# Performance work log

Measured on AMD Instinct MI355X. Metric: run time of the kernel, lower is better.

Reference implementation:

```python
import jax, jax.numpy as jnp
import numpy as np

B, T, C, H, L, V = 4, 1024, 768, 12, 6, 50257
HS = C // H
FF = 4 * C
NEG = jnp.float32(-1e9)


def setup_inputs() -> dict:
    key = jax.random.key(0)
    ks = jax.random.split(key, 16)
    n = lambda k, shape: jax.random.normal(k, shape, jnp.float32) * 0.02
    return {
        "idx": jax.random.randint(ks[0], (B, T), 0, V),
        "targets": jax.random.randint(ks[1], (B, T), 0, V),
        "tok_emb": n(ks[2], (V, C)),
        "pos_emb": n(ks[3], (T, C)),  # block_size == T
        "Wq": n(ks[4], (L, C, C)), "Wk": n(ks[5], (L, C, C)), "Wv": n(ks[6], (L, C, C)),
        "Wp": n(ks[7], (L, C, C)), "bp": jnp.zeros((L, C), jnp.float32),
        "ln1_g": jnp.ones((L, C), jnp.float32), "ln1_b": jnp.zeros((L, C), jnp.float32),
        "ln2_g": jnp.ones((L, C), jnp.float32), "ln2_b": jnp.zeros((L, C), jnp.float32),
        "W1": n(ks[8], (L, C, FF)), "b1": jnp.zeros((L, FF), jnp.float32),
        "W2": n(ks[9], (L, FF, C)), "b2": jnp.zeros((L, C), jnp.float32),
        "lnf_g": jnp.ones((C,), jnp.float32), "lnf_b": jnp.zeros((C,), jnp.float32),
        "Wh": n(ks[10], (C, V)), "bh": jnp.zeros((V,), jnp.float32),
    }


def _ln(x, g, b):
    m = x.mean(-1, keepdims=True)
    v = x.var(-1, keepdims=True)
    return (x - m) * jax.lax.rsqrt(v + 1e-5) * g + b


def reference(idx, targets, tok_emb, pos_emb, Wq, Wk, Wv, Wp, bp,
              ln1_g, ln1_b, ln2_g, ln2_b, W1, b1, W2, b2,
              lnf_g, lnf_b, Wh, bh):
    x = tok_emb[idx] + pos_emb[:T]                       # (B,T,C)
    mask = jnp.tril(jnp.ones((T, T), bool))              # causal tril buffer
    scale = jnp.float32(HS) ** -0.5
    for l in range(L):
        h = _ln(x, ln1_g[l], ln1_b[l])
        q = (h @ Wq[l]).reshape(B, T, H, HS)
        k = (h @ Wk[l]).reshape(B, T, H, HS)
        v = (h @ Wv[l]).reshape(B, T, H, HS)
        wei = jnp.einsum('bihd,bjhd->bhij', q, k) * scale
        wei = jnp.where(mask, wei, NEG)
        wei = jax.nn.softmax(wei, axis=-1)               # dropout is eval no-op
        att = jnp.einsum('bhij,bjhd->bihd', wei, v).reshape(B, T, C)
        x = x + att @ Wp[l] + bp[l]
        h2 = _ln(x, ln2_g[l], ln2_b[l])
        x = x + jax.nn.relu(h2 @ W1[l] + b1[l]) @ W2[l] + b2[l]
    x = _ln(x, lnf_g, lnf_b)
    logits = x @ Wh + bh                                  # (B,T,V)
    logp = jax.nn.log_softmax(logits.reshape(B * T, V), axis=-1)
    nll = -jnp.take_along_axis(logp, targets.reshape(B * T, 1), axis=1)
    loss = nll.mean()
    return logits, loss
```

## Files before the change

kernel.cpp:

```cpp
#include <hip/hip_runtime.h>
#include <hip/hip_bf16.h>

#define DI __device__ __forceinline__

typedef __bf16 bf16_t;
typedef __bf16 bf16x8 __attribute__((ext_vector_type(8)));
typedef float f32x4 __attribute__((ext_vector_type(4)));

static constexpr int Bc = 4, Tc = 1024, Cc = 768, Hc = 12, Lc = 6, Vc = 50257;
static constexpr int FFc = 3072, BT = Bc * Tc;
static constexpr int Vpad = 50304;
static constexpr int NPAN = Vpad / 128;

DI void gld_lds16(const void* g, void* l) {
  __builtin_amdgcn_global_load_lds((__attribute__((address_space(1))) void*)(void*)g,
                                   (__attribute__((address_space(3))) void*)l, 16, 0, 0);
}
DI bf16_t f2b(float v) { return (bf16_t)v; }
DI unsigned short b2u(bf16_t h) { union { bf16_t b; unsigned short u; } x; x.b = h; return x.u; }

__global__ void tconv(const float* __restrict__ src, bf16_t* __restrict__ dst,
                      const int K, const int N, const long sStride, const long dStride) {
  __shared__ float t[32][33];
  src += (long)blockIdx.z * sStride;
  dst += (long)blockIdx.z * dStride;
  const int n0 = blockIdx.x * 32, k0 = blockIdx.y * 32;
  const int tr = threadIdx.x >> 5, tc = threadIdx.x & 31;
#pragma unroll
  for (int i = 0; i < 4; ++i) {
    const int n = n0 + tc;
    t[tr + i * 8][tc] = (n < N) ? src[(long)(k0 + tr + i * 8) * N + n] : 0.f;
  }
  __syncthreads();
#pragma unroll
  for (int i = 0; i < 4; ++i)
    dst[(long)(n0 + tr + i * 8) * K + k0 + tc] = f2b(t[tc][tr + i * 8]);
}

__global__ void embed_ln(const int* __restrict__ idx, const float* __restrict__ tok,
                         const float* __restrict__ pos, const float* __restrict__ g,
                         const float* __restrict__ b, float* __restrict__ X,
                         bf16_t* __restrict__ out) {
  const int lane = threadIdx.x & 63;
  const long row = (long)blockIdx.x * 4 + (threadIdx.x >> 6);
  const int t = (int)(row & (Tc - 1));
  const float* tr = tok + (long)idx[row] * Cc;
  const float* pr = pos + (long)t * Cc;
  float v[12];
  float s = 0.f;
#pragma unroll
  for (int i = 0; i < 3; ++i) {
    const int c = lane * 4 + i * 256;
    const float4 a = *(const float4*)(tr + c);
    const float4 p = *(const float4*)(pr + c);
    float4 x;
    x.x = a.x + p.x; x.y = a.y + p.y; x.z = a.z + p.z; x.w = a.w + p.w;
    *(float4*)(X + row * Cc + c) = x;
    v[i * 4 + 0] = x.x; v[i * 4 + 1] = x.y; v[i * 4 + 2] = x.z; v[i * 4 + 3] = x.w;
    s += x.x + x.y + x.z + x.w;
  }
#pragma unroll
  for (int o = 1; o < 64; o <<= 1) s += __shfl_xor(s, o);
  const float mean = s * (1.f / 768.f);
  float q = 0.f;
#pragma unroll
  for (int j = 0; j < 12; ++j) { const float d = v[j] - mean; q += d * d; }
#pragma unroll
  for (int o = 1; o < 64; o <<= 1) q += __shfl_xor(q, o);
  const float rstd = rsqrtf(q * (1.f / 768.f) + 1e-5f);
#pragma unroll
  for (int i = 0; i < 3; ++i) {
    const int c = lane * 4 + i * 256;
    const float4 gg = *(const float4*)(g + c);
    const float4 bb = *(const float4*)(b + c);
    ushort4 o4;
    o4.x = b2u(f2b((v[i * 4 + 0] - mean) * rstd * gg.x + bb.x));
    o4.y = b2u(f2b((v[i * 4 + 1] - mean) * rstd * gg.y + bb.y));
    o4.z = b2u(f2b((v[i * 4 + 2] - mean) * rstd * gg.z + bb.z));
    o4.w = b2u(f2b((v[i * 4 + 3] - mean) * rstd * gg.w + bb.w));
    *(ushort4*)(out + row * Cc + c) = o4;
  }
}

__global__ void ln_k(const float* __restrict__ x, const float* __restrict__ g,
                     const float* __restrict__ b, bf16_t* __restrict__ out) {
  const int lane = threadIdx.x & 63;
  const long row = (long)blockIdx.x * 4 + (threadIdx.x >> 6);
  const float* xr = x + row * Cc;
  float v[12];
  float s = 0.f;
#pragma unroll
  for (int i = 0; i < 3; ++i) {
    const float4 f = *(const float4*)(xr + lane * 4 + i * 256);
    v[i * 4 + 0] = f.x; v[i * 4 + 1] = f.y; v[i * 4 + 2] = f.z; v[i * 4 + 3] = f.w;
    s += f.x + f.y + f.z + f.w;
  }
#pragma unroll
  for (int o = 1; o < 64; o <<= 1) s += __shfl_xor(s, o);
  const float mean = s * (1.f / 768.f);
  float q = 0.f;
#pragma unroll
  for (int j = 0; j < 12; ++j) { const float d = v[j] - mean; q += d * d; }
#pragma unroll
  for (int o = 1; o < 64; o <<= 1) q += __shfl_xor(q, o);
  const float rstd = rsqrtf(q * (1.f / 768.f) + 1e-5f);
#pragma unroll
  for (int i = 0; i < 3; ++i) {
    const int c = lane * 4 + i * 256;
    const float4 gg = *(const float4*)(g + c);
    const float4 bb = *(const float4*)(b + c);
    ushort4 o4;
    o4.x = b2u(f2b((v[i * 4 + 0] - mean) * rstd * gg.x + bb.x));
    o4.y = b2u(f2b((v[i * 4 + 1] - mean) * rstd * gg.y + bb.y));
    o4.z = b2u(f2b((v[i * 4 + 2] - mean) * rstd * gg.z + bb.z));
    o4.w = b2u(f2b((v[i * 4 + 3] - mean) * rstd * gg.w + bb.w));
    *(ushort4*)(out + row * Cc + c) = o4;
  }
}

__global__ void red_ln(const float* __restrict__ P, const float* __restrict__ bias,
                       const float* __restrict__ g, const float* __restrict__ b,
                       float* __restrict__ X, bf16_t* __restrict__ out) {
  const int lane = threadIdx.x & 63;
  const long row = (long)blockIdx.x * 4 + (threadIdx.x >> 6);
  float v[12];
  float s = 0.f;
#pragma unroll
  for (int i = 0; i < 3; ++i) {
    const int c = lane * 4 + i * 256;
    const float4 x0 = *(const float4*)(X + row * Cc + c);
    const float4 p0 = *(const float4*)(P + row * Cc + c);
    const float4 p1 = *(const float4*)(P + (size_t)BT * Cc + row * Cc + c);
    const float4 bb = *(const float4*)(bias + c);
    float4 x;
    x.x = x0.x + p0.x + p1.x + bb.x;
    x.y = x0.y + p0.y + p1.y + bb.y;
    x.z = x0.z + p0.z + p1.z + bb.z;
    x.w = x0.w + p0.w + p1.w + bb.w;
    *(float4*)(X + row * Cc + c) = x;
    v[i * 4 + 0] = x.x; v[i * 4 + 1] = x.y; v[i * 4 + 2] = x.z; v[i * 4 + 3] = x.w;
    s += x.x + x.y + x.z + x.w;
  }
#pragma unroll
  for (int o = 1; o < 64; o <<= 1) s += __shfl_xor(s, o);
  const float mean = s * (1.f / 768.f);
  float q = 0.f;
#pragma unroll
  for (int j = 0; j < 12; ++j) { const float d = v[j] - mean; q += d * d; }
#pragma unroll
  for (int o = 1; o < 64; o <<= 1) q += __shfl_xor(q, o);
  const float rstd = rsqrtf(q * (1.f / 768.f) + 1e-5f);
#pragma unroll
  for (int i = 0; i < 3; ++i) {
    const int c = lane * 4 + i * 256;
    const float4 gg = *(const float4*)(g + c);
    const float4 bb = *(const float4*)(b + c);
    ushort4 o4;
    o4.x = b2u(f2b((v[i * 4 + 0] - mean) * rstd * gg.x + bb.x));
    o4.y = b2u(f2b((v[i * 4 + 1] - mean) * rstd * gg.y + bb.y));
    o4.z = b2u(f2b((v[i * 4 + 2] - mean) * rstd * gg.z + bb.z));
    o4.w = b2u(f2b((v[i * 4 + 3] - mean) * rstd * gg.w + bb.w));
    *(ushort4*)(out + row * Cc + c) = o4;
  }
}

template <int EPI>
__launch_bounds__(256, 4)
__global__ void gemm_bt(const bf16_t* __restrict__ A, const bf16_t* __restrict__ Bt,
                        const float* __restrict__ bias, bf16_t* __restrict__ outB,
                        float* __restrict__ resid, float* __restrict__ fpart,
                        const int N, const int K, const int ldk, const int ldo) {
  __shared__ __align__(16) bf16_t As[128 * 64];
  __shared__ __align__(16) bf16_t Bs[128 * 64];
  const int tid = threadIdx.x;
  const int lane = tid & 63, wid = tid >> 6;
  const int l4 = lane >> 4, l15 = lane & 15;
  const int wr = wid >> 1, wc = wid & 1;

  int flat;
  {
    const int nwg = gridDim.x * gridDim.y;
    int f = (int)blockIdx.y * gridDim.x + (int)blockIdx.x;
    const int q = nwg >> 3, r = nwg & 7;
    const int xcd = f & 7, pos = f >> 3;
    flat = (xcd < r) ? xcd * (q + 1) + pos : r * (q + 1) + (xcd - r) * q + pos;
  }
  const long m0 = (long)(flat / gridDim.x) * 128;
  const long n0 = (long)(flat % gridDim.x) * 128;
  const long koff = (long)blockIdx.z * K;

  const bf16_t* Ag = A + m0 * ldk + koff;
  const bf16_t* Bg = Bt + n0 * ldk + koff;
  const int srow = tid >> 3, scol = tid & 7;

  f32x4 acc[4][4];
#pragma unroll
  for (int m = 0; m < 4; ++m)
#pragma unroll
    for (int n = 0; n < 4; ++n) acc[m][n] = (f32x4){0.f, 0.f, 0.f, 0.f};

  const int nkt = K >> 6;
  for (int kt = 0; kt < nkt; ++kt) {
    const int kb = kt << 6;
#pragma unroll
    for (int i = 0; i < 4; ++i) {
      const int r_ = i * 32 + srow;
      const int c8 = scol ^ (r_ & 7);
      gld_lds16(Ag + (long)r_ * ldk + kb + c8 * 8, As + (i * 256 + tid) * 8);
      gld_lds16(Bg + (long)r_ * ldk + kb + c8 * 8, Bs + (i * 256 + tid) * 8);
    }
    __syncthreads();
#pragma unroll
    for (int kk = 0; kk < 2; ++kk) {
      bf16x8 af[4], bfv[4];
#pragma unroll
      for (int m = 0; m < 4; ++m) {
        const int row = wr * 64 + m * 16 + l15;
        af[m] = *(const bf16x8*)((const char*)As +
                 ((row * 128 + kk * 64 + l4 * 16) ^ ((row & 7) << 4)));
      }
#pragma unroll
      for (int n = 0; n < 4; ++n) {
        const int row = wc * 64 + n * 16 + l15;
        bfv[n] = *(const bf16x8*)((const char*)Bs +
                 ((row * 128 + kk * 64 + l4 * 16) ^ ((row & 7) << 4)));
      }
#pragma unroll
      for (int m = 0; m < 4; ++m)
#pragma unroll
        for (int n = 0; n < 4; ++n)
          acc[m][n] = __builtin_amdgcn_mfma_f32_16x16x32_bf16(af[m], bfv[n], acc[m][n], 0, 0, 0);
    }
    __syncthreads();
  }

#pragma unroll
  for (int m = 0; m < 4; ++m) {
    const long rowb = m0 + wr * 64 + m * 16 + l4 * 4;
#pragma unroll
    for (int n = 0; n < 4; ++n) {
      const int col = (int)n0 + wc * 64 + n * 16 + l15;
#pragma unroll
      for (int r = 0; r < 4; ++r) {
        const float v = acc[m][n][r];
        const long row = rowb + r;
        if constexpr (EPI == 0) {
          outB[row * ldo + col] = f2b(v);
        } else if constexpr (EPI == 1) {
          const float z = v + bias[col];
          outB[row * ldo + col] = f2b(z > 0.f ? z : 0.f);
        } else if constexpr (EPI == 2) {
          resid[row * ldo + col] += v + bias[col];
        } else {
          fpart[((size_t)blockIdx.z * BT + row) * ldo + col] = v;
        }
      }
    }
  }
}

__launch_bounds__(256, 4)
__global__ void head_k(const bf16_t* __restrict__ A, const bf16_t* __restrict__ Bt,
                       const float* __restrict__ bias, float* __restrict__ outF,
                       const int K, const int ldo, float* __restrict__ part1) {
  __shared__ __align__(16) bf16_t As[128 * 64];
  __shared__ __align__(16) bf16_t Bs[128 * 64];
  const int tid = threadIdx.x;
  const int lane = tid & 63, wid = tid >> 6;
  const int l4 = lane >> 4, l15 = lane & 15;
  const int wr = wid >> 1, wc = wid & 1;
  const long m0 = (long)blockIdx.y * 128;
  const long n0 = (long)blockIdx.x * 128;

  const bf16_t* Ag = A + m0 * K;
  const bf16_t* Bg = Bt + n0 * K;
  const int srow = tid >> 3, scol = tid & 7;

  f32x4 acc[4][4];
#pragma unroll
  for (int m = 0; m < 4; ++m)
#pragma unroll
    for (int n = 0; n < 4; ++n) acc[m][n] = (f32x4){0.f, 0.f, 0.f, 0.f};

  const int nkt = K >> 6;
  for (int kt = 0; kt < nkt; ++kt) {
    const int kb = kt << 6;
#pragma unroll
    for (int i = 0; i < 4; ++i) {
      const int r_ = i * 32 + srow;
      const int c8 = scol ^ (r_ & 7);
      gld_lds16(Ag + (long)r_ * K + kb + c8 * 8, As + (i * 256 + tid) * 8);
      gld_lds16(Bg + (long)r_ * K + kb + c8 * 8, Bs + (i * 256 + tid) * 8);
    }
    __syncthreads();
#pragma unroll
    for (int kk = 0; kk < 2; ++kk) {
      bf16x8 af[4], bfv[4];
#pragma unroll
      for (int m = 0; m < 4; ++m) {
        const int row = wr * 64 + m * 16 + l15;
        af[m] = *(const bf16x8*)((const char*)As +
                 ((row * 128 + kk * 64 + l4 * 16) ^ ((row & 7) << 4)));
      }
#pragma unroll
      for (int n = 0; n < 4; ++n) {
        const int row = wc * 64 + n * 16 + l15;
        bfv[n] = *(const bf16x8*)((const char*)Bs +
                 ((row * 128 + kk * 64 + l4 * 16) ^ ((row & 7) << 4)));
      }
#pragma unroll
      for (int m = 0; m < 4; ++m)
#pragma unroll
        for (int n = 0; n < 4; ++n)
          acc[m][n] = __builtin_amdgcn_mfma_f32_16x16x32_bf16(af[m], bfv[n], acc[m][n], 0, 0, 0);
    }
    __syncthreads();
  }

  float* ps = (float*)&As[0];
#pragma unroll
  for (int m = 0; m < 4; ++m)
#pragma unroll
    for (int r = 0; r < 4; ++r) {
      float s = 0.f;
#pragma unroll
      for (int n = 0; n < 4; ++n) {
        const int col = (int)n0 + wc * 64 + n * 16 + l15;
        s += (col < Vc) ? __expf(acc[m][n][r] + bias[col]) : 0.f;
      }
      ps[(wr * 64 + m * 16 + l4 * 4 + r) * 33 + wc * 16 + l15] = s;
    }
  __syncthreads();
  if (tid < 128) {
    float S = 0.f;
#pragma unroll
    for (int j = 0; j < 32; ++j) S += ps[tid * 33 + j];
    part1[(m0 + tid) * NPAN + (int)(n0 >> 7)] = S;
  }

#pragma unroll
  for (int m = 0; m < 4; ++m) {
    const long rowb = m0 + wr * 64 + m * 16 + l4 * 4;
#pragma unroll
    for (int n = 0; n < 4; ++n) {
      const int col = (int)n0 + wc * 64 + n * 16 + l15;
#pragma unroll
      for (int r = 0; r < 4; ++r)
        if (col < Vc) outF[(rowb + r) * (long)ldo + col] = acc[m][n][r] + bias[col];
    }
  }
}

__launch_bounds__(256, 2)
__global__ void attn_k(const bf16_t* __restrict__ qkv, bf16_t* __restrict__ att) {
  const int qt = blockIdx.x;
  const int bh = blockIdx.y;
  const int b = bh / Hc, h = bh % Hc;
  const int tid = threadIdx.x;
  const int lane = tid & 63, wid = tid >> 6;
  const int l4 = lane >> 4, l15 = lane & 15;

  __shared__ __align__(16) bf16_t Ks[64 * 64];
  __shared__ __align__(16) bf16_t Vt[64 * 72];
  __shared__ __align__(16) bf16_t Ps[4][16 * 64];

  const long qrow0 = (long)b * Tc + qt * 64 + wid * 16;
  bf16x8 qf0, qf1;
  {
    const bf16_t* qp = qkv + (qrow0 + l15) * 2304 + h * 64 + l4 * 8;
    qf0 = *(const bf16x8*)qp;
    qf1 = *(const bf16x8*)(qp + 32);
  }
  f32x4 oacc[4];
#pragma unroll
  for (int f = 0; f < 4; ++f) oacc[f] = (f32x4){0.f, 0.f, 0.f, 0.f};
  float mrow[4] = {-3.0e38f, -3.0e38f, -3.0e38f, -3.0e38f};
  float lrw[4] = {0.f, 0.f, 0.f, 0.f};

  for (int kt = 0; kt <= qt; ++kt) {
    const long kvb = (long)b * Tc + kt * 64;
#pragma unroll
    for (int i = 0; i < 2; ++i) {
      const int c = i * 256 + tid;
      const int r_ = c >> 3;
      const int c8 = (c & 7) ^ (r_ & 7);
      gld_lds16(qkv + (kvb + r_) * 2304 + Cc + h * 64 + c8 * 8, Ks + (size_t)c * 8);
    }
    {
      const int kv = tid >> 2;
      const int d0 = (tid & 3) * 16;
      const bf16_t* vp = qkv + (kvb + kv) * 2304 + 2 * Cc + h * 64 + d0;
      const bf16x8 v0 = *(const bf16x8*)vp;
      const bf16x8 v1 = *(const bf16x8*)(vp + 8);
#pragma unroll
      for (int j = 0; j < 8; ++j) Vt[(d0 + j) * 72 + kv] = v0[j];
#pragma unroll
      for (int j = 0; j < 8; ++j) Vt[(d0 + 8 + j) * 72 + kv] = v1[j];
    }
    __syncthreads();

    f32x4 sf[4];
#pragma unroll
    for (int f = 0; f < 4; ++f) {
      const int row = f * 16 + l15;
      const bf16x8 kb0 = *(const bf16x8*)((const char*)Ks +
                        ((row * 128 + l4 * 16) ^ ((row & 7) << 4)));
      const bf16x8 kb1 = *(const bf16x8*)((const char*)Ks +
                        ((row * 128 + 64 + l4 * 16) ^ ((row & 7) << 4)));
      f32x4 z = (f32x4){0.f, 0.f, 0.f, 0.f};
      z = __builtin_amdgcn_mfma_f32_16x16x32_bf16(qf0, kb0, z, 0, 0, 0);
      sf[f] = __builtin_amdgcn_mfma_f32_16x16x32_bf16(qf1, kb1, z, 0, 0, 0);
    }
    float alpha[4];
#pragma unroll
    for (int r = 0; r < 4; ++r) {
      const int qpos = qt * 64 + wid * 16 + l4 * 4 + r;
      float mx = -3.0e38f;
#pragma unroll
      for (int f = 0; f < 4; ++f) {
        const int kpos = kt * 64 + f * 16 + l15;
        float sv = sf[f][r] * 0.125f;
        sv = (kpos <= qpos) ? sv : -1e9f;
        sf[f][r] = sv;
        mx = fmaxf(mx, sv);
      }
      mx = fmaxf(mx, __shfl_xor(mx, 1));
      mx = fmaxf(mx, __shfl_xor(mx, 2));
      mx = fmaxf(mx, __shfl_xor(mx, 4));
      mx = fmaxf(mx, __shfl_xor(mx, 8));
      const float mn = fmaxf(mrow[r], mx);
      alpha[r] = __expf(mrow[r] - mn);
      mrow[r] = mn;
      float rs = 0.f;
#pragma unroll
      for (int f = 0; f < 4; ++f) {
        const float pw = __expf(sf[f][r] - mn);
        sf[f][r] = pw;
        rs += pw;
      }
      rs += __shfl_xor(rs, 1); rs += __shfl_xor(rs, 2);
      rs += __shfl_xor(rs, 4); rs += __shfl_xor(rs, 8);
      lrw[r] = lrw[r] * alpha[r] + rs;
    }
    char* pb = (char*)&Ps[wid][0];
#pragma unroll
    for (int r = 0; r < 4; ++r) {
      const int i_ = l4 * 4 + r;
#pragma unroll
      for (int f = 0; f < 4; ++f) {
        const int j_ = f * 16 + l15;
        *(bf16_t*)(pb + ((i_ * 128 + j_ * 2) ^ ((i_ & 7) << 4))) = f2b(sf[f][r]);
      }
    }
#pragma unroll
    for (int f = 0; f < 4; ++f)
#pragma unroll
      for (int r = 0; r < 4; ++r) oacc[f][r] *= alpha[r];

    bf16x8 pa0, pa1;
    {
      const int row = l15;
      pa0 = *(const bf16x8*)(pb + ((row * 128 + l4 * 16) ^ ((row & 7) << 4)));
      pa1 = *(const bf16x8*)(pb + ((row * 128 + 64 + l4 * 16) ^ ((row & 7) << 4)));
    }
#pragma unroll
    for (int f = 0; f < 4; ++f) {
      const bf16_t* vb0 = Vt + (f * 16 + l15) * 72 + l4 * 8;
      oacc[f] = __builtin_amdgcn_mfma_f32_16x16x32_bf16(pa0, *(const bf16x8*)vb0, oacc[f], 0, 0, 0);
      oacc[f] = __builtin_amdgcn_mfma_f32_16x16x32_bf16(pa1, *(const bf16x8*)(vb0 + 32), oacc[f], 0, 0, 0);
    }
    __syncthreads();
  }
#pragma unroll
  for (int f = 0; f < 4; ++f) {
    const int col = h * 64 + f * 16 + l15;
#pragma unroll
    for (int r = 0; r < 4; ++r) {
      const long row = qrow0 + l4 * 4 + r;
      att[row * Cc + col] = f2b(oacc[f][r] / lrw[r]);
    }
  }
}

__global__ void loss_rows(const float* __restrict__ p1, const float* __restrict__ logits,
                          const int* __restrict__ tgt, float* __restrict__ part) {
  const int row = blockIdx.x * 4 + (threadIdx.x >> 6);
  const int lane = threadIdx.x & 63;
  float S = 0.f;
  for (int i = lane; i < NPAN; i += 64) S += p1[(long)row * NPAN + i];
#pragma unroll
  for (int o = 1; o < 64; o <<= 1) S += __shfl_xor(S, o);
  if (lane == 0)
    part[row] = logf(S) - logits[(long)row * Vc + tgt[row]];
}

__global__ void loss_final(const float* __restrict__ part, float* __restrict__ out) {
  float s = 0.f;
  for (int i = threadIdx.x; i < BT; i += 256) s += part[i];
#pragma unroll
  for (int o = 1; o < 64; o <<= 1) s += __shfl_xor(s, o);
  __shared__ float sw[4];
  const int wid = threadIdx.x >> 6;
  if ((threadIdx.x & 63) == 0) sw[wid] = s;
  __syncthreads();
  if (threadIdx.x == 0) out[0] = (sw[0] + sw[1] + sw[2] + sw[3]) / (float)BT;
}

extern "C" void kernel_launch(void* const* d_in, const int* in_sizes, int n_in,
                              void* d_out, int out_size, void* d_ws, size_t ws_size,
                              hipStream_t stream) {
  (void)in_sizes; (void)n_in; (void)out_size; (void)ws_size;
  const int* idx = (const int*)d_in[0];
  const int* tgt = (const int*)d_in[1];
  const float* tok = (const float*)d_in[2];
  const float* pos = (const float*)d_in[3];
  const float* Wq = (const float*)d_in[4];
  const float* Wk = (const float*)d_in[5];
  const float* Wv = (const float*)d_in[6];
  const float* Wp = (const float*)d_in[7];
  const float* bp = (const float*)d_in[8];
  const float* ln1g = (const float*)d_in[9];
  const float* ln1b = (const float*)d_in[10];
  const float* ln2g = (const float*)d_in[11];
  const float* ln2b = (const float*)d_in[12];
  const float* W1 = (const float*)d_in[13];
  const float* b1 = (const float*)d_in[14];
  const float* W2 = (const float*)d_in[15];
  const float* b2 = (const float*)d_in[16];
  const float* lnfg = (const float*)d_in[17];
  const float* lnfb = (const float*)d_in[18];
  const float* Wh = (const float*)d_in[19];
  const float* bh = (const float*)d_in[20];

  char* p = (char*)d_ws;
  auto take = [&](size_t bytes) { char* r = p; p += (bytes + 255) & ~(size_t)255; return r; };
  bf16_t* WTQKV = (bf16_t*)take((size_t)Lc * 2304 * Cc * 2);
  bf16_t* WTP   = (bf16_t*)take((size_t)Lc * Cc * Cc * 2);
  bf16_t* WT1   = (bf16_t*)take((size_t)Lc * FFc * Cc * 2);
  bf16_t* WT2   = (bf16_t*)take((size_t)Lc * Cc * FFc * 2);
  bf16_t* WTH   = (bf16_t*)take((size_t)Vpad * Cc * 2);
  float*  X     = (float*)take((size_t)BT * Cc * 4);
  bf16_t* Hb    = (bf16_t*)take((size_t)BT * Cc * 2);
  bf16_t* QKVb  = (bf16_t*)take((size_t)BT * 2304 * 2);
  bf16_t* ATT   = (bf16_t*)take((size_t)BT * Cc * 2);
  bf16_t* FFb   = (bf16_t*)take((size_t)BT * FFc * 2);
  float*  FPART = (float*)QKVb;
  float*  PART1 = (float*)FFb;
  float*  PART  = (float*)ATT;

  tconv<<<dim3(24, 24, Lc), 256, 0, stream>>>(Wq, WTQKV, Cc, Cc, (long)Cc * Cc, (long)2304 * Cc);
  tconv<<<dim3(24, 24, Lc), 256, 0, stream>>>(Wk, WTQKV + (size_t)Cc * Cc, Cc, Cc, (long)Cc * Cc, (long)2304 * Cc);
  tconv<<<dim3(24, 24, Lc), 256, 0, stream>>>(Wv, WTQKV + (size_t)2 * Cc * Cc, Cc, Cc, (long)Cc * Cc, (long)2304 * Cc);
  tconv<<<dim3(24, 24, Lc), 256, 0, stream>>>(Wp, WTP, Cc, Cc, (long)Cc * Cc, (long)Cc * Cc);
  tconv<<<dim3(96, 24, Lc), 256, 0, stream>>>(W1, WT1, Cc, FFc, (long)Cc * FFc, (long)FFc * Cc);
  tconv<<<dim3(24, 96, Lc), 256, 0, stream>>>(W2, WT2, FFc, Cc, (long)FFc * Cc, (long)Cc * FFc);
  tconv<<<dim3(Vpad / 32, 24, 1), 256, 0, stream>>>(Wh, WTH, Cc, Vc, 0, 0);

  embed_ln<<<BT / 4, 256, 0, stream>>>(idx, tok, pos, ln1g, ln1b, X, Hb);

  for (int l = 0; l < Lc; ++l) {
    const bf16_t* wqkv = WTQKV + (size_t)l * 2304 * Cc;
    const bf16_t* wp   = WTP + (size_t)l * Cc * Cc;
    const bf16_t* w1   = WT1 + (size_t)l * FFc * Cc;
    const bf16_t* w2   = WT2 + (size_t)l * Cc * FFc;
    gemm_bt<0><<<dim3(18, 32), 256, 0, stream>>>(Hb, wqkv, nullptr, QKVb, nullptr, nullptr, 2304, Cc, Cc, 2304);
    attn_k<<<dim3(Tc / 64, Bc * Hc), 256, 0, stream>>>(QKVb, ATT);
    gemm_bt<2><<<dim3(6, 32), 256, 0, stream>>>(ATT, wp, bp + (size_t)l * Cc, nullptr, X, nullptr, Cc, Cc, Cc, Cc);
    ln_k<<<BT / 4, 256, 0, stream>>>(X, ln2g + (size_t)l * Cc, ln2b + (size_t)l * Cc, Hb);
    gemm_bt<1><<<dim3(24, 32), 256, 0, stream>>>(Hb, w1, b1 + (size_t)l * FFc, FFb, nullptr, nullptr, FFc, Cc, Cc, FFc);
    gemm_bt<4><<<dim3(6, 32, 2), 256, 0, stream>>>(FFb, w2, nullptr, nullptr, nullptr, FPART, Cc, FFc / 2, FFc, Cc);
    const float* gN = (l + 1 < Lc) ? ln1g + (size_t)(l + 1) * Cc : lnfg;
    const float* bN = (l + 1 < Lc) ? ln1b + (size_t)(l + 1) * Cc : lnfb;
    red_ln<<<BT / 4, 256, 0, stream>>>(FPART, b2 + (size_t)l * Cc, gN, bN, X, Hb);
  }
  head_k<<<dim3(NPAN, 32), 256, 0, stream>>>(Hb, WTH, bh, (float*)d_out, Cc, Vc, PART1);
  loss_rows<<<BT / 4, 256, 0, stream>>>(PART1, (const float*)d_out, tgt, PART);
  loss_final<<<1, 256, 0, stream>>>(PART, (float*)d_out + (size_t)BT * Vc);
}
```

Baseline: 1.915 ms.

## Emit transposed V from QKV GEMM and split-K the attention projection

The QKV GEMM epilogue now writes the V columns straight into a transposed VT buffer. The attention kernel can then load V tiles into swizzled LDS with async global-to-LDS copies, replacing the per-element transpose scatter, and its occupancy bound rises from 2 to 3. The output projection switches to a split-K GEMM with fp32 partials, and red_ln reduces them while adding the bias and residual and applying LN2. This removes the separate ln_k and the read-modify-write residual epilogue, at the cost of extra partial-buffer traffic and a new VT workspace.

```diff
diff --git a/kernel.cpp b/kernel.cpp
--- a/kernel.cpp
+++ b/kernel.cpp
@@ -58,42 +58,6 @@
     *(float4*)(X + row * Cc + c) = x;
     v[i * 4 + 0] = x.x; v[i * 4 + 1] = x.y; v[i * 4 + 2] = x.z; v[i * 4 + 3] = x.w;
     s += x.x + x.y + x.z + x.w;
-  }
-#pragma unroll
-  for (int o = 1; o < 64; o <<= 1) s += __shfl_xor(s, o);
-  const float mean = s * (1.f / 768.f);
-  float q = 0.f;
-#pragma unroll
-  for (int j = 0; j < 12; ++j) { const float d = v[j] - mean; q += d * d; }
-#pragma unroll
-  for (int o = 1; o < 64; o <<= 1) q += __shfl_xor(q, o);
-  const float rstd = rsqrtf(q * (1.f / 768.f) + 1e-5f);
-#pragma unroll
-  for (int i = 0; i < 3; ++i) {
-    const int c = lane * 4 + i * 256;
-    const float4 gg = *(const float4*)(g + c);
-    const float4 bb = *(const float4*)(b + c);
-    ushort4 o4;
-    o4.x = b2u(f2b((v[i * 4 + 0] - mean) * rstd * gg.x + bb.x));
-    o4.y = b2u(f2b((v[i * 4 + 1] - mean) * rstd * gg.y + bb.y));
-    o4.z = b2u(f2b((v[i * 4 + 2] - mean) * rstd * gg.z + bb.z));
-    o4.w = b2u(f2b((v[i * 4 + 3] - mean) * rstd * gg.w + bb.w));
-    *(ushort4*)(out + row * Cc + c) = o4;
-  }
-}
-
-__global__ void ln_k(const float* __restrict__ x, const float* __restrict__ g,
-                     const float* __restrict__ b, bf16_t* __restrict__ out) {
-  const int lane = threadIdx.x & 63;
-  const long row = (long)blockIdx.x * 4 + (threadIdx.x >> 6);
-  const float* xr = x + row * Cc;
-  float v[12];
-  float s = 0.f;
-#pragma unroll
-  for (int i = 0; i < 3; ++i) {
-    const float4 f = *(const float4*)(xr + lane * 4 + i * 256);
-    v[i * 4 + 0] = f.x; v[i * 4 + 1] = f.y; v[i * 4 + 2] = f.z; v[i * 4 + 3] = f.w;
-    s += f.x + f.y + f.z + f.w;
   }
 #pragma unroll
   for (int o = 1; o < 64; o <<= 1) s += __shfl_xor(s, o);
@@ -168,7 +132,7 @@
 __launch_bounds__(256, 4)
 __global__ void gemm_bt(const bf16_t* __restrict__ A, const bf16_t* __restrict__ Bt,
                         const float* __restrict__ bias, bf16_t* __restrict__ outB,
-                        float* __restrict__ resid, float* __restrict__ fpart,
+                        bf16_t* __restrict__ vtr, float* __restrict__ fpart,
                         const int N, const int K, const int ldk, const int ldo) {
   __shared__ __align__(16) bf16_t As[128 * 64];
   __shared__ __align__(16) bf16_t Bs[128 * 64];
@@ -234,6 +198,25 @@
     __syncthreads();
   }
 
+  if constexpr (EPI == 5) {
+    if ((int)n0 >= 1536) {
+#pragma unroll
+      for (int m = 0; m < 4; ++m) {
+        const long rowb = m0 + wr * 64 + m * 16 + l4 * 4;
+#pragma unroll
+        for (int n = 0; n < 4; ++n) {
+          const int col = (int)n0 + wc * 64 + n * 16 + l15;
+          ushort4 w;
+          w.x = b2u(f2b(acc[m][n][0]));
+          w.y = b2u(f2b(acc[m][n][1]));
+          w.z = b2u(f2b(acc[m][n][2]));
+          w.w = b2u(f2b(acc[m][n][3]));
+          *(ushort4*)(vtr + (size_t)(col - 1536) * BT + rowb) = w;
+        }
+      }
+      return;
+    }
+  }
 #pragma unroll
   for (int m = 0; m < 4; ++m) {
     const long rowb = m0 + wr * 64 + m * 16 + l4 * 4;
@@ -244,13 +227,11 @@
       for (int r = 0; r < 4; ++r) {
         const float v = acc[m][n][r];
         const long row = rowb + r;
-        if constexpr (EPI == 0) {
+        if constexpr (EPI == 0 || EPI == 5) {
           outB[row * ldo + col] = f2b(v);
         } else if constexpr (EPI == 1) {
           const float z = v + bias[col];
           outB[row * ldo + col] = f2b(z > 0.f ? z : 0.f);
-        } else if constexpr (EPI == 2) {
-          resid[row * ldo + col] += v + bias[col];
         } else {
           fpart[((size_t)blockIdx.z * BT + row) * ldo + col] = v;
         }
@@ -351,8 +332,9 @@
   }
 }
 
-__launch_bounds__(256, 2)
-__global__ void attn_k(const bf16_t* __restrict__ qkv, bf16_t* __restrict__ att) {
+__launch_bounds__(256, 3)
+__global__ void attn_k(const bf16_t* __restrict__ qkv, const bf16_t* __restrict__ vt,
+                       bf16_t* __restrict__ att) {
   const int qt = blockIdx.x;
   const int bh = blockIdx.y;
   const int b = bh / Hc, h = bh % Hc;
@@ -361,7 +343,7 @@
   const int l4 = lane >> 4, l15 = lane & 15;
 
   __shared__ __align__(16) bf16_t Ks[64 * 64];
-  __shared__ __align__(16) bf16_t Vt[64 * 72];
+  __shared__ __align__(16) bf16_t Vts[64 * 64];
   __shared__ __align__(16) bf16_t Ps[4][16 * 64];
 
   const long qrow0 = (long)b * Tc + qt * 64 + wid * 16;
@@ -386,16 +368,12 @@
       const int c8 = (c & 7) ^ (r_ & 7);
       gld_lds16(qkv + (kvb + r_) * 2304 + Cc + h * 64 + c8 * 8, Ks + (size_t)c * 8);
     }
-    {
-      const int kv = tid >> 2;
-      const int d0 = (tid & 3) * 16;
-      const bf16_t* vp = qkv + (kvb + kv) * 2304 + 2 * Cc + h * 64 + d0;
-      const bf16x8 v0 = *(const bf16x8*)vp;
-      const bf16x8 v1 = *(const bf16x8*)(vp + 8);
-#pragma unroll
-      for (int j = 0; j < 8; ++j) Vt[(d0 + j) * 72 + kv] = v0[j];
-#pragma unroll
-      for (int j = 0; j < 8; ++j) Vt[(d0 + 8 + j) * 72 + kv] = v1[j];
+#pragma unroll
+    for (int i = 0; i < 2; ++i) {
+      const int c = i * 256 + tid;
+      const int r_ = c >> 3;
+      const int c8 = (c & 7) ^ (r_ & 7);
+      gld_lds16(vt + (size_t)(h * 64 + r_) * BT + kvb + c8 * 8, Vts + (size_t)c * 8);
     }
     __syncthreads();
 
@@ -465,9 +443,13 @@
     }
 #pragma unroll
     for (int f = 0; f < 4; ++f) {
-      const bf16_t* vb0 = Vt + (f * 16 + l15) * 72 + l4 * 8;
-      oacc[f] = __builtin_amdgcn_mfma_f32_16x16x32_bf16(pa0, *(const bf16x8*)vb0, oacc[f], 0, 0, 0);
-      oacc[f] = __builtin_amdgcn_mfma_f32_16x16x32_bf16(pa1, *(const bf16x8*)(vb0 + 32), oacc[f], 0, 0, 0);
+      const int row = f * 16 + l15;
+      const bf16x8 vb0 = *(const bf16x8*)((const char*)Vts +
+                        ((row * 128 + l4 * 16) ^ ((row & 7) << 4)));
+      const bf16x8 vb1 = *(const bf16x8*)((const char*)Vts +
+                        ((row * 128 + 64 + l4 * 16) ^ ((row & 7) << 4)));
+      oacc[f] = __builtin_amdgcn_mfma_f32_16x16x32_bf16(pa0, vb0, oacc[f], 0, 0, 0);
+      oacc[f] = __builtin_amdgcn_mfma_f32_16x16x32_bf16(pa1, vb1, oacc[f], 0, 0, 0);
     }
     __syncthreads();
   }
@@ -544,6 +526,8 @@
   bf16_t* QKVb  = (bf16_t*)take((size_t)BT * 2304 * 2);
   bf16_t* ATT   = (bf16_t*)take((size_t)BT * Cc * 2);
   bf16_t* FFb   = (bf16_t*)take((size_t)BT * FFc * 2);
+  bf16_t* VT    = (bf16_t*)take((size_t)BT * Cc * 2);
+  float*  FPROJ = (float*)take((size_t)2 * BT * Cc * 4);
   float*  FPART = (float*)QKVb;
   float*  PART1 = (float*)FFb;
   float*  PART  = (float*)ATT;
@@ -563,10 +547,10 @@
     const bf16_t* wp   = WTP + (size_t)l * Cc * Cc;
     const bf16_t* w1   = WT1 + (size_t)l * FFc * Cc;
     const bf16_t* w2   = WT2 + (size_t)l * Cc * FFc;
-    gemm_bt<0><<<dim3(18, 32), 256, 0, stream>>>(Hb, wqkv, nullptr, QKVb, nullptr, nullptr, 2304, Cc, Cc, 2304);
-    attn_k<<<dim3(Tc / 64, Bc * Hc), 256, 0, stream>>>(QKVb, ATT);
-    gemm_bt<2><<<dim3(6, 32), 256, 0, stream>>>(ATT, wp, bp + (size_t)l * Cc, nullptr, X, nullptr, Cc, Cc, Cc, Cc);
-    ln_k<<<BT / 4, 256, 0, stream>>>(X, ln2g + (size_t)l * Cc, ln2b + (size_t)l * Cc, Hb);
+    gemm_bt<5><<<dim3(18, 32), 256, 0, stream>>>(Hb, wqkv, nullptr, QKVb, VT, nullptr, 2304, Cc, Cc, 2304);
+    attn_k<<<dim3(Tc / 64, Bc * Hc), 256, 0, stream>>>(QKVb, VT, ATT);
+    gemm_bt<4><<<dim3(6, 32, 2), 256, 0, stream>>>(ATT, wp, nullptr, nullptr, nullptr, FPROJ, Cc, Cc / 2, Cc, Cc);
+    red_ln<<<BT / 4, 256, 0, stream>>>(FPROJ, bp + (size_t)l * Cc, ln2g + (size_t)l * Cc, ln2b + (size_t)l * Cc, X, Hb);
     gemm_bt<1><<<dim3(24, 32), 256, 0, stream>>>(Hb, w1, b1 + (size_t)l * FFc, FFb, nullptr, nullptr, FFc, Cc, Cc, FFc);
     gemm_bt<4><<<dim3(6, 32, 2), 256, 0, stream>>>(FFb, w2, nullptr, nullptr, nullptr, FPART, Cc, FFc / 2, FFc, Cc);
     const float* gN = (l + 1 < Lc) ? ln1g + (size_t)(l + 1) * Cc : lnfg;
```

Result: faster. 1.777 ms (-7.2%).
